# Performance work log

Hardware: AMD Instinct MI355X
Metric: run time of the kernel (lower is better)

The kernel has to match this reference:

```python
import jax, jax.numpy as jnp
import numpy as np

ALPHA = 0.2      # GAT leaky_relu slope (args.alpha)
MLP_SLOPE = 0.01 # F.leaky_relu default in the MLP path
NEG = -9e15

def _l2_normalize(x, axis=1, eps=1e-12):
    n = jnp.sqrt(jnp.sum(x * x, axis=axis, keepdims=True))
    return x / jnp.maximum(n, eps)

def setup_inputs() -> dict:
    key = jax.random.key(0)
    ks = jax.random.split(key, 14)
    N, Din, Dh, H, Dg, M1, M2, E = 8192, 512, 256, 2, 512, 512, 256, 100000
    x = jax.random.normal(ks[0], (N, Din), dtype=jnp.float32)
    adj = jax.random.randint(ks[1], (N, N), 0, 2, dtype=jnp.int32)
    train_sample = jax.random.randint(ks[2], (E, 2), 0, N, dtype=jnp.int32)
    llm_emb = jax.random.normal(ks[3], (N, Dg), dtype=jnp.float32)
    # GAT head params (stacked over heads)
    Wg = jax.random.normal(ks[4], (H, Din, Dh), dtype=jnp.float32) * 0.05
    a1 = jax.random.normal(ks[5], (H, Dh), dtype=jnp.float32) * 0.05
    a2 = jax.random.normal(ks[6], (H, Dh), dtype=jnp.float32) * 0.05
    bias_g = jnp.zeros((H, Dh), dtype=jnp.float32)
    # MLP params
    W1 = jax.random.normal(ks[7], (Dh + Dg, M1), dtype=jnp.float32) * 0.03
    b1 = jnp.zeros((M1,), dtype=jnp.float32)
    W2 = jax.random.normal(ks[8], (M1, M2), dtype=jnp.float32) * 0.04
    b2 = jnp.zeros((M2,), dtype=jnp.float32)
    return {"x": x, "adj": adj, "train_sample": train_sample, "llm_emb": llm_emb,
            "Wg": Wg, "a1": a1, "a2": a2, "bias_g": bias_g,
            "W1": W1, "b1": b1, "W2": W2, "b2": b2}

def reference(x, adj, train_sample, llm_emb, Wg, a1, a2, bias_g, W1, b1, W2, b2):
    mask = adj > 0  # [N, N]

    def head(W, av1, av2, b):
        h = x @ W                                   # [N, Dh]
        s1 = h @ av1                                # [N]
        s2 = h @ av2                                # [N]
        e = jax.nn.leaky_relu(s1[:, None] + s2[None, :], ALPHA)  # [N, N]
        att = jax.nn.softmax(jnp.where(mask, e, NEG), axis=1)
        out = att @ h                               # [N, Dh]
        out = jax.nn.leaky_relu(out, ALPHA)
        out = _l2_normalize(out, axis=1)
        return out + b

    # encode: single GNN layer -> mean over heads (dropout inactive in eval)
    out_heads = jax.vmap(head)(Wg, a1, a2, bias_g)  # [H, N, Dh]
    embed_gnn = jnp.mean(out_heads, axis=0)         # [N, Dh]
    embed = jnp.concatenate([llm_emb, embed_gnn], axis=1)  # [N, Dg+Dh]

    def mlp(z):
        z = jax.nn.leaky_relu(z @ W1 + b1, MLP_SLOPE)
        z = jax.nn.leaky_relu(z @ W2 + b2, MLP_SLOPE)
        return z

    tf_embed = mlp(embed)
    target_embed = mlp(embed)
    train_tf = tf_embed[train_sample[:, 0]]
    train_tg = target_embed[train_sample[:, 1]]
    pred = jnp.sum(train_tf * train_tg, axis=1, keepdims=True)  # dot decode, [E,1]
    return pred
```

## Files before the change

kernel.cpp:

```cpp
#include <hip/hip_runtime.h>
#include <hip/hip_bf16.h>
#include <cstdint>
#include <cstddef>

#define ALPHA 0.2f
#define MLP_SLOPE 0.01f

typedef short bf16x8 __attribute__((ext_vector_type(8)));
typedef float f32x4 __attribute__((ext_vector_type(4)));
typedef unsigned short ushort_t;

__device__ __forceinline__ float lrelu(float x, float s) { return x > 0.f ? x : x * s; }
__device__ __forceinline__ ushort_t f2bf(float x) {
  __hip_bfloat16 h = __float2bfloat16(x);
  return *reinterpret_cast<ushort_t*>(&h);
}
__device__ __forceinline__ float bf2f(ushort_t u) {
  union { unsigned int i; float f; } v; v.i = ((unsigned int)u) << 16; return v.f;
}

__global__ __launch_bounds__(256) void split_f(
    const float* __restrict__ in, ushort_t* __restrict__ hi,
    ushort_t* __restrict__ lo)
{
  int idx = blockIdx.x * 256 + threadIdx.x;
  float4 v = ((const float4*)in)[idx];
  ushort4 h, l;
  h.x = f2bf(v.x); l.x = f2bf(v.x - bf2f(h.x));
  h.y = f2bf(v.y); l.y = f2bf(v.y - bf2f(h.y));
  h.z = f2bf(v.z); l.z = f2bf(v.z - bf2f(h.z));
  h.w = f2bf(v.w); l.w = f2bf(v.w - bf2f(h.w));
  ((ushort4*)hi)[idx] = h;
  ((ushort4*)lo)[idx] = l;
}

__global__ __launch_bounds__(256) void split_t(
    const float* __restrict__ W, ushort_t* __restrict__ Thi,
    ushort_t* __restrict__ Tlo, int K, int N)
{
  int idx = blockIdx.x * 256 + threadIdx.x;
  if (idx >= K * N) return;
  int k = idx / N, n = idx - k * N;
  size_t b = (size_t)blockIdx.y * K * N;
  float v = W[b + idx];
  ushort_t h = f2bf(v);
  size_t o = b + (size_t)n * K + k;
  Thi[o] = h; Tlo[o] = f2bf(v - bf2f(h));
}

__global__ __launch_bounds__(256, 2) void gemm_bf16s(
    const ushort_t* __restrict__ Ahi, const ushort_t* __restrict__ Alo,
    const ushort_t* __restrict__ Bthi, const ushort_t* __restrict__ Btlo,
    const float* __restrict__ bias, float* __restrict__ Cf,
    ushort_t* __restrict__ Chi, ushort_t* __restrict__ Clo,
    int M, int N, int K, float slope, int act)
{
  __shared__ ushort_t Ah[128][40], Al[128][40], Bh[128][40], Bl[128][40];
  const size_t boff = (size_t)blockIdx.z * N * K;
  const size_t coff = (size_t)blockIdx.z * M * N;
  const int t = threadIdx.x;
  const int m0 = blockIdx.y * 128, n0 = blockIdx.x * 128;
  const int srow = t >> 1, spart = (t & 1) * 16;
  const int wave = t >> 6;
  const int wm = (wave >> 1) * 64, wn = (wave & 1) * 64;
  const int l16 = t & 15, quad = (t >> 4) & 3;
  f32x4 acc[4][4];
#pragma unroll
  for (int i = 0; i < 4; ++i)
#pragma unroll
    for (int j = 0; j < 4; ++j) acc[i][j] = (f32x4){0.f, 0.f, 0.f, 0.f};

  for (int k0 = 0; k0 < K; k0 += 32) {
    __syncthreads();
    const size_t abase = (size_t)(m0 + srow) * K + k0 + spart;
    const size_t bbase = boff + (size_t)(n0 + srow) * K + k0 + spart;
    *(uint4*)&Ah[srow][spart]     = *(const uint4*)&Ahi[abase];
    *(uint4*)&Ah[srow][spart + 8] = *(const uint4*)&Ahi[abase + 8];
    *(uint4*)&Al[srow][spart]     = *(const uint4*)&Alo[abase];
    *(uint4*)&Al[srow][spart + 8] = *(const uint4*)&Alo[abase + 8];
    *(uint4*)&Bh[srow][spart]     = *(const uint4*)&Bthi[bbase];
    *(uint4*)&Bh[srow][spart + 8] = *(const uint4*)&Bthi[bbase + 8];
    *(uint4*)&Bl[srow][spart]     = *(const uint4*)&Btlo[bbase];
    *(uint4*)&Bl[srow][spart + 8] = *(const uint4*)&Btlo[bbase + 8];
    __syncthreads();
    bf16x8 afh[4], afl[4], bfh[4], bfl[4];
#pragma unroll
    for (int mt = 0; mt < 4; ++mt) {
      afh[mt] = *(const bf16x8*)&Ah[wm + mt * 16 + l16][quad * 8];
      afl[mt] = *(const bf16x8*)&Al[wm + mt * 16 + l16][quad * 8];
    }
#pragma unroll
    for (int nt = 0; nt < 4; ++nt) {
      bfh[nt] = *(const bf16x8*)&Bh[wn + nt * 16 + l16][quad * 8];
      bfl[nt] = *(const bf16x8*)&Bl[wn + nt * 16 + l16][quad * 8];
    }
#pragma unroll
    for (int mt = 0; mt < 4; ++mt)
#pragma unroll
      for (int nt = 0; nt < 4; ++nt) {
        acc[mt][nt] = __builtin_amdgcn_mfma_f32_16x16x32_bf16(afh[mt], bfh[nt], acc[mt][nt], 0, 0, 0);
        acc[mt][nt] = __builtin_amdgcn_mfma_f32_16x16x32_bf16(afh[mt], bfl[nt], acc[mt][nt], 0, 0, 0);
        acc[mt][nt] = __builtin_amdgcn_mfma_f32_16x16x32_bf16(afl[mt], bfh[nt], acc[mt][nt], 0, 0, 0);
      }
  }
#pragma unroll
  for (int mt = 0; mt < 4; ++mt)
#pragma unroll
    for (int nt = 0; nt < 4; ++nt)
#pragma unroll
      for (int rg = 0; rg < 4; ++rg) {
        int m = m0 + wm + mt * 16 + quad * 4 + rg;
        int n = n0 + wn + nt * 16 + l16;
        float v = acc[mt][nt][rg];
        if (bias) v += bias[n];
        if (act) v = lrelu(v, slope);
        size_t o = coff + (size_t)m * N + n;
        if (Cf) Cf[o] = v;
        if (Chi) {
          ushort_t h = f2bf(v);
          Chi[o] = h; Clo[o] = f2bf(v - bf2f(h));
        }
      }
}

__global__ __launch_bounds__(256) void s_kernel(
    const float* __restrict__ hbuf, const float* __restrict__ a1,
    const float* __restrict__ a2, float* __restrict__ s1, float* __restrict__ s2)
{
  const int gw = (blockIdx.x * 256 + threadIdx.x) >> 6;
  const int lane = threadIdx.x & 63;
#pragma unroll
  for (int hh = 0; hh < 2; ++hh) {
    float4 hv = ((const float4*)(hbuf + ((size_t)hh * 8192 + gw) * 256))[lane];
    float4 a1v = ((const float4*)(a1 + hh * 256))[lane];
    float4 a2v = ((const float4*)(a2 + hh * 256))[lane];
    float p1 = hv.x * a1v.x + hv.y * a1v.y + hv.z * a1v.z + hv.w * a1v.w;
    float p2 = hv.x * a2v.x + hv.y * a2v.y + hv.z * a2v.z + hv.w * a2v.w;
    for (int off = 32; off > 0; off >>= 1) {
      p1 += __shfl_xor(p1, off);
      p2 += __shfl_xor(p2, off);
    }
    if (lane == 0) {
      s1[hh * 8192 + gw] = p1;
      s2[hh * 8192 + gw] = p2;
    }
  }
}

__global__ __launch_bounds__(256) void h_pack(
    const float* __restrict__ hbuf, ushort_t* __restrict__ Bpack)
{
  int gid = blockIdx.x * 256 + threadIdx.x;
  int lane = gid & 63;
  int ntile = (gid >> 6) & 15;
  int kblk = (gid >> 10) & 255;
  int head = gid >> 18;
  int c = ntile * 16 + (lane & 15);
  int jb = kblk * 32 + (lane >> 4) * 8;
  ushort_t o[8];
#pragma unroll
  for (int e = 0; e < 8; ++e)
    o[e] = f2bf(hbuf[((size_t)head * 8192 + jb + e) * 256 + c]);
  *(uint4*)&Bpack[(size_t)gid * 8] = *(uint4*)o;
}

__global__ __launch_bounds__(256, 2) void attn_mfma2(
    const ushort_t* __restrict__ Bpack, const float* __restrict__ s1g,
    const float* __restrict__ s2g, const int* __restrict__ adj,
    ushort_t* __restrict__ pacc, float* __restrict__ pl)
{
  __shared__ ushort_t Wlds[2][2][4][64][8];
  const int t = threadIdx.x;
  const int i0 = blockIdx.x * 64;
  const int js = blockIdx.y;
  const int kbase = js * 2048;
  const int wr = t >> 2, kq = t & 3;
  const int glane = kq * 16 + (wr & 15);
  const int gmt = wr >> 4;
  const float s1v0 = s1g[i0 + wr];
  const float s1v1 = s1g[8192 + i0 + wr];
  const int wave = t >> 6, head = wave >> 1, nh = wave & 1;
  const int l16 = t & 15, quad = (t >> 4) & 3;
  const int l63 = t & 63;
  f32x4 acc[4][8];
#pragma unroll
  for (int m = 0; m < 4; ++m)
#pragma unroll
    for (int n = 0; n < 8; ++n) acc[m][n] = (f32x4){0.f, 0.f, 0.f, 0.f};
  float rs0 = 0.f, rs1 = 0.f;

  const int* arow = adj + (size_t)(i0 + wr) * 8192;
  int4 pa0, pa1;
  float4 p20a, p20b, p21a, p21b;
  {
    const int kk = kbase + kq * 8;
    pa0 = *(const int4*)&arow[kk];
    pa1 = *(const int4*)&arow[kk + 4];
    p20a = *(const float4*)&s2g[kk];
    p20b = *(const float4*)&s2g[kk + 4];
    p21a = *(const float4*)&s2g[8192 + kk];
    p21b = *(const float4*)&s2g[8192 + kk + 4];
  }
  for (int kt = 0; kt < 64; ++kt) {
    const int buf = kt & 1;
    {
      int am[8] = {pa0.x, pa0.y, pa0.z, pa0.w, pa1.x, pa1.y, pa1.z, pa1.w};
      float s20[8] = {p20a.x, p20a.y, p20a.z, p20a.w, p20b.x, p20b.y, p20b.z, p20b.w};
      float s21[8] = {p21a.x, p21a.y, p21a.z, p21a.w, p21b.x, p21b.y, p21b.z, p21b.w};
      ushort_t w0[8], w1[8];
#pragma unroll
      for (int e = 0; e < 8; ++e) {
        float e0 = s1v0 + s20[e];
        float e1 = s1v1 + s21[e];
        e0 = fmaxf(e0, 0.f) + ALPHA * fminf(e0, 0.f);
        e1 = fmaxf(e1, 0.f) + ALPHA * fminf(e1, 0.f);
        float v0 = am[e] > 0 ? __expf(e0) : 0.f;
        float v1 = am[e] > 0 ? __expf(e1) : 0.f;
        rs0 += v0; rs1 += v1;
        w0[e] = f2bf(v0); w1[e] = f2bf(v1);
      }
      *(uint4*)&Wlds[buf][0][gmt][glane][0] = *(uint4*)w0;
      *(uint4*)&Wlds[buf][1][gmt][glane][0] = *(uint4*)w1;
    }
    if (kt < 63) {
      const int kk = kbase + (kt + 1) * 32 + kq * 8;
      pa0 = *(const int4*)&arow[kk];
      pa1 = *(const int4*)&arow[kk + 4];
      p20a = *(const float4*)&s2g[kk];
      p20b = *(const float4*)&s2g[kk + 4];
      p21a = *(const float4*)&s2g[8192 + kk];
      p21b = *(const float4*)&s2g[8192 + kk + 4];
    }
    __syncthreads();
    const int kblk = js * 64 + kt;
    const ushort_t* bbase =
        Bpack + ((((size_t)head * 256 + kblk) * 16 + nh * 8) * 64 + l63) * 8;
    bf16x8 Af[4], Bf[8];
#pragma unroll
    for (int mt = 0; mt < 4; ++mt)
      Af[mt] = *(const bf16x8*)&Wlds[buf][head][mt][l63][0];
#pragma unroll
    for (int nt = 0; nt < 8; ++nt)
      Bf[nt] = *(const bf16x8*)&bbase[nt * 512];
#pragma unroll
    for (int mt = 0; mt < 4; ++mt)
#pragma unroll
      for (int nt = 0; nt < 8; ++nt)
        acc[mt][nt] = __builtin_amdgcn_mfma_f32_16x16x32_bf16(
            Af[mt], Bf[nt], acc[mt][nt], 0, 0, 0);
  }
  rs0 += __shfl_xor(rs0, 1); rs0 += __shfl_xor(rs0, 2);
  rs1 += __shfl_xor(rs1, 1); rs1 += __shfl_xor(rs1, 2);
  if (kq == 0) {
    pl[((size_t)js * 2 + 0) * 8192 + i0 + wr] = rs0;
    pl[((size_t)js * 2 + 1) * 8192 + i0 + wr] = rs1;
  }
  const int n0 = nh * 128;
#pragma unroll
  for (int mt = 0; mt < 4; ++mt)
#pragma unroll
    for (int nt = 0; nt < 8; ++nt)
#pragma unroll
      for (int rg = 0; rg < 4; ++rg) {
        int row = i0 + mt * 16 + quad * 4 + rg;
        int col = n0 + nt * 16 + l16;
        pacc[(((size_t)js * 2 + head) * 8192 + row) * 256 + col] =
            f2bf(acc[mt][nt][rg]);
      }
}

__global__ __launch_bounds__(256) void attn_finalize(
    const ushort_t* __restrict__ pacc, const float* __restrict__ pl,
    const float* __restrict__ bg, float* __restrict__ embed)
{
  __shared__ float red[256];
  const int r = blockIdx.x;
  const int t = threadIdx.x;
  float o[2], nrm[2];
#pragma unroll
  for (int hh = 0; hh < 2; ++hh) {
    float num = 0.f, l = 0.f;
#pragma unroll
    for (int js = 0; js < 4; ++js) {
      num += bf2f(pacc[(((size_t)js * 2 + hh) * 8192 + r) * 256 + t]);
      l += pl[((size_t)js * 2 + hh) * 8192 + r];
    }
    o[hh] = lrelu(num / l, ALPHA);
  }
  for (int hh = 0; hh < 2; ++hh) {
    __syncthreads();
    red[t] = o[hh] * o[hh];
    __syncthreads();
    for (int s = 128; s > 0; s >>= 1) {
      if (t < s) red[t] += red[t + s];
      __syncthreads();
    }
    nrm[hh] = fmaxf(sqrtf(red[0]), 1e-12f);
  }
  embed[(size_t)r * 768 + 512 + t] =
      0.5f * (o[0] / nrm[0] + bg[t] + o[1] / nrm[1] + bg[256 + t]);
}

__global__ __launch_bounds__(256) void copy_llm(
    const float* __restrict__ llm, float* __restrict__ embed)
{
  int idx = blockIdx.x * 256 + threadIdx.x;
  int r = idx >> 7, c = idx & 127;
  ((float4*)embed)[(size_t)r * 192 + c] = ((const float4*)llm)[idx];
}

__global__ __launch_bounds__(256) void pred_kernel(
    const float* __restrict__ z2, const int* __restrict__ ts,
    float* __restrict__ out, int E)
{
  const int gw = (blockIdx.x * 256 + threadIdx.x) >> 6;
  const int lane = threadIdx.x & 63;
  if (gw >= E) return;
  const int a = ts[gw * 2], b = ts[gw * 2 + 1];
  float4 va = ((const float4*)(z2 + (size_t)a * 256))[lane];
  float4 vb = ((const float4*)(z2 + (size_t)b * 256))[lane];
  float p = va.x * vb.x + va.y * vb.y + va.z * vb.z + va.w * vb.w;
  for (int off = 32; off > 0; off >>= 1) p += __shfl_xor(p, off);
  if (lane == 0) out[gw] = p;
}

extern "C" void kernel_launch(void* const* d_in, const int* in_sizes, int n_in,
                              void* d_out, int out_size, void* d_ws, size_t ws_size,
                              hipStream_t stream) {
  const float* x   = (const float*)d_in[0];
  const int*   adj = (const int*)d_in[1];
  const int*   ts  = (const int*)d_in[2];
  const float* llm = (const float*)d_in[3];
  const float* Wg  = (const float*)d_in[4];
  const float* a1  = (const float*)d_in[5];
  const float* a2  = (const float*)d_in[6];
  const float* bg  = (const float*)d_in[7];
  const float* W1  = (const float*)d_in[8];
  const float* b1  = (const float*)d_in[9];
  const float* W2  = (const float*)d_in[10];
  const float* b2  = (const float*)d_in[11];
  float* out = (float*)d_out;
  float* ws  = (float*)d_ws;
  const int E = in_sizes[2] / 2;

  float*    hbuf  = ws;
  ushort_t* Bpack = (ushort_t*)(ws + 4194304);
  float*    embed = ws;
  ushort_t* xhi   = (ushort_t*)(ws + 6291456);
  ushort_t* xlo   = (ushort_t*)(ws + 8388608);
  ushort_t* z1hi  = xhi;
  ushort_t* z1lo  = xlo;
  float*    s1    = ws + 10485760;
  float*    s2    = ws + 10502144;
  float*    pl    = ws + 10518528;
  ushort_t* pacc  = (ushort_t*)(ws + 10584064);
  ushort_t* ehi   = (ushort_t*)(ws + 10584064);
  ushort_t* elo   = (ushort_t*)(ws + 13729792);
  float*    z2    = ws + 16875520;
  ushort_t* wgthi = (ushort_t*)(ws + 18972672);
  ushort_t* wgtlo = (ushort_t*)(ws + 19103744);
  ushort_t* w1thi = (ushort_t*)(ws + 19234816);
  ushort_t* w1tlo = (ushort_t*)(ws + 19431424);
  ushort_t* w2thi = (ushort_t*)(ws + 19628032);
  ushort_t* w2tlo = (ushort_t*)(ws + 19693568);

  split_f<<<4096, 256, 0, stream>>>(x, xhi, xlo);
  split_t<<<dim3(512, 2), 256, 0, stream>>>(Wg, wgthi, wgtlo, 512, 256);
  split_t<<<dim3(1536, 1), 256, 0, stream>>>(W1, w1thi, w1tlo, 768, 512);
  split_t<<<dim3(512, 1), 256, 0, stream>>>(W2, w2thi, w2tlo, 512, 256);
  gemm_bf16s<<<dim3(2, 64, 2), 256, 0, stream>>>(
      xhi, xlo, wgthi, wgtlo, nullptr, hbuf, nullptr, nullptr,
      8192, 256, 512, 0.f, 0);
  s_kernel<<<2048, 256, 0, stream>>>(hbuf, a1, a2, s1, s2);
  h_pack<<<2048, 256, 0, stream>>>(hbuf, Bpack);
  attn_mfma2<<<dim3(128, 4), 256, 0, stream>>>(Bpack, s1, s2, adj, pacc, pl);
  copy_llm<<<4096, 256, 0, stream>>>(llm, embed);
  attn_finalize<<<8192, 256, 0, stream>>>(pacc, pl, bg, embed);
  split_f<<<6144, 256, 0, stream>>>(embed, ehi, elo);
  gemm_bf16s<<<dim3(4, 64, 1), 256, 0, stream>>>(
      ehi, elo, w1thi, w1tlo, b1, nullptr, z1hi, z1lo,
      8192, 512, 768, MLP_SLOPE, 1);
  gemm_bf16s<<<dim3(2, 64, 1), 256, 0, stream>>>(
      z1hi, z1lo, w2thi, w2tlo, b2, z2, nullptr, nullptr,
      8192, 256, 512, MLP_SLOPE, 1);
  pred_kernel<<<(E * 64 + 255) / 256, 256, 0, stream>>>(z2, ts, out, E);
}
```

Baseline: 667.8 us.

## Compute attention weights in registers, halve GEMM N-tile, fuse llm copy into finalize

The attention kernel now builds each lane's MFMA A-fragment directly in registers from its own adjacency rows, so the LDS staging buffer and the per-iteration __syncthreads are gone. The cost is that each head's waves compute exp values separately, and the two column-half waves of a head repeat the same work. The split-bf16 GEMM moves to a 128x64 tile with padded LDS rows, doubling the grid size. The llm_emb copy is folded into attn_finalize to save one launch.

```diff
diff --git a/kernel.cpp b/kernel.cpp
--- a/kernel.cpp
+++ b/kernel.cpp
@@ -55,49 +55,62 @@
     ushort_t* __restrict__ Chi, ushort_t* __restrict__ Clo,
     int M, int N, int K, float slope, int act)
 {
-  __shared__ ushort_t Ah[128][40], Al[128][40], Bh[128][40], Bl[128][40];
+  __shared__ ushort_t Ah[128][42], Al[128][42], Bh[64][42], Bl[64][42];
   const size_t boff = (size_t)blockIdx.z * N * K;
   const size_t coff = (size_t)blockIdx.z * M * N;
   const int t = threadIdx.x;
-  const int m0 = blockIdx.y * 128, n0 = blockIdx.x * 128;
-  const int srow = t >> 1, spart = (t & 1) * 16;
+  const int m0 = blockIdx.y * 128, n0 = blockIdx.x * 64;
   const int wave = t >> 6;
-  const int wm = (wave >> 1) * 64, wn = (wave & 1) * 64;
+  const int wm = (wave & 1) * 64, wn = (wave >> 1) * 32;
   const int l16 = t & 15, quad = (t >> 4) & 3;
-  f32x4 acc[4][4];
+  const int tr = t & 127;
+  f32x4 acc[4][2];
 #pragma unroll
   for (int i = 0; i < 4; ++i)
 #pragma unroll
-    for (int j = 0; j < 4; ++j) acc[i][j] = (f32x4){0.f, 0.f, 0.f, 0.f};
+    for (int j = 0; j < 2; ++j) acc[i][j] = (f32x4){0.f, 0.f, 0.f, 0.f};
 
   for (int k0 = 0; k0 < K; k0 += 32) {
     __syncthreads();
-    const size_t abase = (size_t)(m0 + srow) * K + k0 + spart;
-    const size_t bbase = boff + (size_t)(n0 + srow) * K + k0 + spart;
-    *(uint4*)&Ah[srow][spart]     = *(const uint4*)&Ahi[abase];
-    *(uint4*)&Ah[srow][spart + 8] = *(const uint4*)&Ahi[abase + 8];
-    *(uint4*)&Al[srow][spart]     = *(const uint4*)&Alo[abase];
-    *(uint4*)&Al[srow][spart + 8] = *(const uint4*)&Alo[abase + 8];
-    *(uint4*)&Bh[srow][spart]     = *(const uint4*)&Bthi[bbase];
-    *(uint4*)&Bh[srow][spart + 8] = *(const uint4*)&Bthi[bbase + 8];
-    *(uint4*)&Bl[srow][spart]     = *(const uint4*)&Btlo[bbase];
-    *(uint4*)&Bl[srow][spart + 8] = *(const uint4*)&Btlo[bbase + 8];
+    {
+      const size_t abase = (size_t)(m0 + tr) * K + k0;
+      if (t < 128) {
+#pragma unroll
+        for (int j = 0; j < 4; ++j)
+          *(uint4*)&Ah[tr][j * 8] = *(const uint4*)&Ahi[abase + j * 8];
+      } else {
+#pragma unroll
+        for (int j = 0; j < 4; ++j)
+          *(uint4*)&Al[tr][j * 8] = *(const uint4*)&Alo[abase + j * 8];
+        const int br = tr & 63;
+        const size_t bbase = boff + (size_t)(n0 + br) * K + k0;
+        if (tr < 64) {
+#pragma unroll
+          for (int j = 0; j < 4; ++j)
+            *(uint4*)&Bh[br][j * 8] = *(const uint4*)&Bthi[bbase + j * 8];
+        } else {
+#pragma unroll
+          for (int j = 0; j < 4; ++j)
+            *(uint4*)&Bl[br][j * 8] = *(const uint4*)&Btlo[bbase + j * 8];
+        }
+      }
+    }
     __syncthreads();
-    bf16x8 afh[4], afl[4], bfh[4], bfl[4];
+    bf16x8 afh[4], afl[4], bfh[2], bfl[2];
 #pragma unroll
     for (int mt = 0; mt < 4; ++mt) {
       afh[mt] = *(const bf16x8*)&Ah[wm + mt * 16 + l16][quad * 8];
       afl[mt] = *(const bf16x8*)&Al[wm + mt * 16 + l16][quad * 8];
     }
 #pragma unroll
-    for (int nt = 0; nt < 4; ++nt) {
+    for (int nt = 0; nt < 2; ++nt) {
       bfh[nt] = *(const bf16x8*)&Bh[wn + nt * 16 + l16][quad * 8];
       bfl[nt] = *(const bf16x8*)&Bl[wn + nt * 16 + l16][quad * 8];
     }
 #pragma unroll
     for (int mt = 0; mt < 4; ++mt)
 #pragma unroll
-      for (int nt = 0; nt < 4; ++nt) {
+      for (int nt = 0; nt < 2; ++nt) {
         acc[mt][nt] = __builtin_amdgcn_mfma_f32_16x16x32_bf16(afh[mt], bfh[nt], acc[mt][nt], 0, 0, 0);
         acc[mt][nt] = __builtin_amdgcn_mfma_f32_16x16x32_bf16(afh[mt], bfl[nt], acc[mt][nt], 0, 0, 0);
         acc[mt][nt] = __builtin_amdgcn_mfma_f32_16x16x32_bf16(afl[mt], bfh[nt], acc[mt][nt], 0, 0, 0);
@@ -106,7 +119,7 @@
 #pragma unroll
   for (int mt = 0; mt < 4; ++mt)
 #pragma unroll
-    for (int nt = 0; nt < 4; ++nt)
+    for (int nt = 0; nt < 2; ++nt)
 #pragma unroll
       for (int rg = 0; rg < 4; ++rg) {
         int m = m0 + wm + mt * 16 + quad * 4 + rg;
@@ -164,84 +177,91 @@
   *(uint4*)&Bpack[(size_t)gid * 8] = *(uint4*)o;
 }
 
-__global__ __launch_bounds__(256, 2) void attn_mfma2(
+__global__ __launch_bounds__(256, 2) void attn_mfma3(
     const ushort_t* __restrict__ Bpack, const float* __restrict__ s1g,
     const float* __restrict__ s2g, const int* __restrict__ adj,
     ushort_t* __restrict__ pacc, float* __restrict__ pl)
 {
-  __shared__ ushort_t Wlds[2][2][4][64][8];
   const int t = threadIdx.x;
   const int i0 = blockIdx.x * 64;
   const int js = blockIdx.y;
   const int kbase = js * 2048;
-  const int wr = t >> 2, kq = t & 3;
-  const int glane = kq * 16 + (wr & 15);
-  const int gmt = wr >> 4;
-  const float s1v0 = s1g[i0 + wr];
-  const float s1v1 = s1g[8192 + i0 + wr];
   const int wave = t >> 6, head = wave >> 1, nh = wave & 1;
-  const int l16 = t & 15, quad = (t >> 4) & 3;
+  const int l16 = t & 15, oct = (t >> 4) & 3;
   const int l63 = t & 63;
+
+  float s1v[4];
+#pragma unroll
+  for (int mt = 0; mt < 4; ++mt)
+    s1v[mt] = s1g[(size_t)head * 8192 + i0 + mt * 16 + l16];
+  const float* s2h = s2g + (size_t)head * 8192;
+
   f32x4 acc[4][8];
 #pragma unroll
   for (int m = 0; m < 4; ++m)
 #pragma unroll
     for (int n = 0; n < 8; ++n) acc[m][n] = (f32x4){0.f, 0.f, 0.f, 0.f};
-  float rs0 = 0.f, rs1 = 0.f;
-
-  const int* arow = adj + (size_t)(i0 + wr) * 8192;
-  int4 pa0, pa1;
-  float4 p20a, p20b, p21a, p21b;
+  float rs[4] = {0.f, 0.f, 0.f, 0.f};
+
+  const int* arow[4];
+#pragma unroll
+  for (int mt = 0; mt < 4; ++mt)
+    arow[mt] = adj + (size_t)(i0 + mt * 16 + l16) * 8192;
+
+  int4 pa0[4], pa1[4];
+  float4 ps2a, ps2b;
   {
-    const int kk = kbase + kq * 8;
-    pa0 = *(const int4*)&arow[kk];
-    pa1 = *(const int4*)&arow[kk + 4];
-    p20a = *(const float4*)&s2g[kk];
-    p20b = *(const float4*)&s2g[kk + 4];
-    p21a = *(const float4*)&s2g[8192 + kk];
-    p21b = *(const float4*)&s2g[8192 + kk + 4];
-  }
+    const int kk = kbase + oct * 8;
+#pragma unroll
+    for (int mt = 0; mt < 4; ++mt) {
+      pa0[mt] = *(const int4*)&arow[mt][kk];
+      pa1[mt] = *(const int4*)&arow[mt][kk + 4];
+    }
+    ps2a = *(const float4*)&s2h[kk];
+    ps2b = *(const float4*)&s2h[kk + 4];
+  }
+
   for (int kt = 0; kt < 64; ++kt) {
-    const int buf = kt & 1;
-    {
-      int am[8] = {pa0.x, pa0.y, pa0.z, pa0.w, pa1.x, pa1.y, pa1.z, pa1.w};
-      float s20[8] = {p20a.x, p20a.y, p20a.z, p20a.w, p20b.x, p20b.y, p20b.z, p20b.w};
-      float s21[8] = {p21a.x, p21a.y, p21a.z, p21a.w, p21b.x, p21b.y, p21b.z, p21b.w};
-      ushort_t w0[8], w1[8];
+    const int kblk = js * 64 + kt;
+    const ushort_t* bb =
+        Bpack + ((((size_t)head * 256 + kblk) * 16 + nh * 8) * 64 + l63) * 8;
+    bf16x8 Bf[8];
+#pragma unroll
+    for (int nt = 0; nt < 8; ++nt)
+      Bf[nt] = *(const bf16x8*)&bb[nt * 512];
+
+    float s2v[8] = {ps2a.x, ps2a.y, ps2a.z, ps2a.w,
+                    ps2b.x, ps2b.y, ps2b.z, ps2b.w};
+    bf16x8 Af[4];
+#pragma unroll
+    for (int mt = 0; mt < 4; ++mt) {
+      int av[8] = {pa0[mt].x, pa0[mt].y, pa0[mt].z, pa0[mt].w,
+                   pa1[mt].x, pa1[mt].y, pa1[mt].z, pa1[mt].w};
+      ushort_t w[8] __attribute__((aligned(16)));
+      float r = 0.f;
 #pragma unroll
       for (int e = 0; e < 8; ++e) {
-        float e0 = s1v0 + s20[e];
-        float e1 = s1v1 + s21[e];
-        e0 = fmaxf(e0, 0.f) + ALPHA * fminf(e0, 0.f);
-        e1 = fmaxf(e1, 0.f) + ALPHA * fminf(e1, 0.f);
-        float v0 = am[e] > 0 ? __expf(e0) : 0.f;
-        float v1 = am[e] > 0 ? __expf(e1) : 0.f;
-        rs0 += v0; rs1 += v1;
-        w0[e] = f2bf(v0); w1[e] = f2bf(v1);
-      }
-      *(uint4*)&Wlds[buf][0][gmt][glane][0] = *(uint4*)w0;
-      *(uint4*)&Wlds[buf][1][gmt][glane][0] = *(uint4*)w1;
-    }
+        float ev = s1v[mt] + s2v[e];
+        ev = fmaxf(ev, 0.f) + ALPHA * fminf(ev, 0.f);
+        float wv = av[e] > 0 ? __expf(ev) : 0.f;
+        r += wv;
+        w[e] = f2bf(wv);
+      }
+      rs[mt] += r;
+      Af[mt] = *(const bf16x8*)w;
+    }
+
     if (kt < 63) {
-      const int kk = kbase + (kt + 1) * 32 + kq * 8;
-      pa0 = *(const int4*)&arow[kk];
-      pa1 = *(const int4*)&arow[kk + 4];
-      p20a = *(const float4*)&s2g[kk];
-      p20b = *(const float4*)&s2g[kk + 4];
-      p21a = *(const float4*)&s2g[8192 + kk];
-      p21b = *(const float4*)&s2g[8192 + kk + 4];
-    }
-    __syncthreads();
-    const int kblk = js * 64 + kt;
-    const ushort_t* bbase =
-        Bpack + ((((size_t)head * 256 + kblk) * 16 + nh * 8) * 64 + l63) * 8;
-    bf16x8 Af[4], Bf[8];
-#pragma unroll
-    for (int mt = 0; mt < 4; ++mt)
-      Af[mt] = *(const bf16x8*)&Wlds[buf][head][mt][l63][0];
-#pragma unroll
-    for (int nt = 0; nt < 8; ++nt)
-      Bf[nt] = *(const bf16x8*)&bbase[nt * 512];
+      const int kk = kbase + (kt + 1) * 32 + oct * 8;
+#pragma unroll
+      for (int mt = 0; mt < 4; ++mt) {
+        pa0[mt] = *(const int4*)&arow[mt][kk];
+        pa1[mt] = *(const int4*)&arow[mt][kk + 4];
+      }
+      ps2a = *(const float4*)&s2h[kk];
+      ps2b = *(const float4*)&s2h[kk + 4];
+    }
+
 #pragma unroll
     for (int mt = 0; mt < 4; ++mt)
 #pragma unroll
@@ -249,12 +269,18 @@
         acc[mt][nt] = __builtin_amdgcn_mfma_f32_16x16x32_bf16(
             Af[mt], Bf[nt], acc[mt][nt], 0, 0, 0);
   }
-  rs0 += __shfl_xor(rs0, 1); rs0 += __shfl_xor(rs0, 2);
-  rs1 += __shfl_xor(rs1, 1); rs1 += __shfl_xor(rs1, 2);
-  if (kq == 0) {
-    pl[((size_t)js * 2 + 0) * 8192 + i0 + wr] = rs0;
-    pl[((size_t)js * 2 + 1) * 8192 + i0 + wr] = rs1;
-  }
+
+#pragma unroll
+  for (int mt = 0; mt < 4; ++mt) {
+    rs[mt] += __shfl_xor(rs[mt], 16);
+    rs[mt] += __shfl_xor(rs[mt], 32);
+  }
+  if (nh == 0 && oct == 0) {
+#pragma unroll
+    for (int mt = 0; mt < 4; ++mt)
+      pl[((size_t)js * 2 + head) * 8192 + i0 + mt * 16 + l16] = rs[mt];
+  }
+
   const int n0 = nh * 128;
 #pragma unroll
   for (int mt = 0; mt < 4; ++mt)
@@ -262,7 +288,7 @@
     for (int nt = 0; nt < 8; ++nt)
 #pragma unroll
       for (int rg = 0; rg < 4; ++rg) {
-        int row = i0 + mt * 16 + quad * 4 + rg;
+        int row = i0 + mt * 16 + oct * 4 + rg;
         int col = n0 + nt * 16 + l16;
         pacc[(((size_t)js * 2 + head) * 8192 + row) * 256 + col] =
             f2bf(acc[mt][nt][rg]);
@@ -271,11 +297,15 @@
 
 __global__ __launch_bounds__(256) void attn_finalize(
     const ushort_t* __restrict__ pacc, const float* __restrict__ pl,
-    const float* __restrict__ bg, float* __restrict__ embed)
+    const float* __restrict__ bg, const float* __restrict__ llm,
+    float* __restrict__ embed)
 {
   __shared__ float red[256];
   const int r = blockIdx.x;
   const int t = threadIdx.x;
+  if (t < 128)
+    *(float4*)&embed[(size_t)r * 768 + t * 4] =
+        *(const float4*)&llm[(size_t)r * 512 + t * 4];
   float o[2], nrm[2];
 #pragma unroll
   for (int hh = 0; hh < 2; ++hh) {
@@ -299,14 +329,6 @@
   }
   embed[(size_t)r * 768 + 512 + t] =
       0.5f * (o[0] / nrm[0] + bg[t] + o[1] / nrm[1] + bg[256 + t]);
-}
-
-__global__ __launch_bounds__(256) void copy_llm(
-    const float* __restrict__ llm, float* __restrict__ embed)
-{
-  int idx = blockIdx.x * 256 + threadIdx.x;
-  int r = idx >> 7, c = idx & 127;
-  ((float4*)embed)[(size_t)r * 192 + c] = ((const float4*)llm)[idx];
 }
 
 __global__ __launch_bounds__(256) void pred_kernel(
@@ -368,19 +390,18 @@
   split_t<<<dim3(512, 2), 256, 0, stream>>>(Wg, wgthi, wgtlo, 512, 256);
   split_t<<<dim3(1536, 1), 256, 0, stream>>>(W1, w1thi, w1tlo, 768, 512);
   split_t<<<dim3(512, 1), 256, 0, stream>>>(W2, w2thi, w2tlo, 512, 256);
-  gemm_bf16s<<<dim3(2, 64, 2), 256, 0, stream>>>(
+  gemm_bf16s<<<dim3(4, 64, 2), 256, 0, stream>>>(
       xhi, xlo, wgthi, wgtlo, nullptr, hbuf, nullptr, nullptr,
       8192, 256, 512, 0.f, 0);
   s_kernel<<<2048, 256, 0, stream>>>(hbuf, a1, a2, s1, s2);
   h_pack<<<2048, 256, 0, stream>>>(hbuf, Bpack);
-  attn_mfma2<<<dim3(128, 4), 256, 0, stream>>>(Bpack, s1, s2, adj, pacc, pl);
-  copy_llm<<<4096, 256, 0, stream>>>(llm, embed);
-  attn_finalize<<<8192, 256, 0, stream>>>(pacc, pl, bg, embed);
+  attn_mfma3<<<dim3(128, 4), 256, 0, stream>>>(Bpack, s1, s2, adj, pacc, pl);
+  attn_finalize<<<8192, 256, 0, stream>>>(pacc, pl, bg, llm, embed);
   split_f<<<6144, 256, 0, stream>>>(embed, ehi, elo);
-  gemm_bf16s<<<dim3(4, 64, 1), 256, 0, stream>>>(
+  gemm_bf16s<<<dim3(8, 64, 1), 256, 0, stream>>>(
       ehi, elo, w1thi, w1tlo, b1, nullptr, z1hi, z1lo,
       8192, 512, 768, MLP_SLOPE, 1);
-  gemm_bf16s<<<dim3(2, 64, 1), 256, 0, stream>>>(
+  gemm_bf16s<<<dim3(4, 64, 1), 256, 0, stream>>>(
       z1hi, z1lo, w2thi, w2tlo, b2, z2, nullptr, nullptr,
       8192, 256, 512, MLP_SLOPE, 1);
   pred_kernel<<<(E * 64 + 255) / 256, 256, 0, stream>>>(z2, ts, out, E);
```

Result: slower. 745.4 us (+11.6%).

## Pre-pack weights into MFMA fragment layout and drop LDS staging in GEMMs

Applied to the files above, without the earlier changes.

Weights are now packed into the per-lane MFMA B-fragment layout, so the split-bf16 GEMM can load A and B fragments straight from global memory into registers with double buffering, without LDS or block barriers. The GEMM tile shrinks to 128x64 per block, which doubles the grid. In the attention kernel the Bpack fragment loads are issued before the weight computation so their latency overlaps it, and __syncthreads is replaced by an inline-asm lgkmcnt wait plus s_barrier. The llm copy kernel is folded into attn_finalize. The risks are uncoalesced global A loads with no LDS reuse across waves, and the asm barrier does not wait on vmcnt.

```diff
diff --git a/kernel.cpp b/kernel.cpp
--- a/kernel.cpp
+++ b/kernel.cpp
@@ -9,6 +9,8 @@
 typedef short bf16x8 __attribute__((ext_vector_type(8)));
 typedef float f32x4 __attribute__((ext_vector_type(4)));
 typedef unsigned short ushort_t;
+
+#define ASM_BARRIER() __asm__ __volatile__("s_waitcnt lgkmcnt(0)\n\ts_barrier" ::: "memory")
 
 __device__ __forceinline__ float lrelu(float x, float s) { return x > 0.f ? x : x * s; }
 __device__ __forceinline__ ushort_t f2bf(float x) {
@@ -34,83 +36,112 @@
   ((ushort4*)lo)[idx] = l;
 }
 
-__global__ __launch_bounds__(256) void split_t(
-    const float* __restrict__ W, ushort_t* __restrict__ Thi,
-    ushort_t* __restrict__ Tlo, int K, int N)
-{
-  int idx = blockIdx.x * 256 + threadIdx.x;
-  if (idx >= K * N) return;
-  int k = idx / N, n = idx - k * N;
+__global__ __launch_bounds__(256) void pack_wt(
+    const float* __restrict__ W, ushort_t* __restrict__ hi,
+    ushort_t* __restrict__ lo, int K, int N)
+{
+  int gid = blockIdx.x * 256 + threadIdx.x;
+  int lane = gid & 63;
+  int kbc = K >> 5;
+  int kblk = (gid >> 6) % kbc;
+  int nblk = (gid >> 6) / kbc;
   size_t b = (size_t)blockIdx.y * K * N;
-  float v = W[b + idx];
-  ushort_t h = f2bf(v);
-  size_t o = b + (size_t)n * K + k;
-  Thi[o] = h; Tlo[o] = f2bf(v - bf2f(h));
-}
-
-__global__ __launch_bounds__(256, 2) void gemm_bf16s(
+  int col = nblk * 16 + (lane & 15);
+  int krow = kblk * 32 + (lane >> 4) * 8;
+  ushort_t h[8] __attribute__((aligned(16)));
+  ushort_t l[8] __attribute__((aligned(16)));
+#pragma unroll
+  for (int e = 0; e < 8; ++e) {
+    float v = W[b + (size_t)(krow + e) * N + col];
+    h[e] = f2bf(v);
+    l[e] = f2bf(v - bf2f(h[e]));
+  }
+  *(uint4*)&hi[b + (size_t)gid * 8] = *(uint4*)h;
+  *(uint4*)&lo[b + (size_t)gid * 8] = *(uint4*)l;
+}
+
+__global__ __launch_bounds__(256) void gemm_nolds(
     const ushort_t* __restrict__ Ahi, const ushort_t* __restrict__ Alo,
-    const ushort_t* __restrict__ Bthi, const ushort_t* __restrict__ Btlo,
+    const ushort_t* __restrict__ Bph, const ushort_t* __restrict__ Bpl,
     const float* __restrict__ bias, float* __restrict__ Cf,
     ushort_t* __restrict__ Chi, ushort_t* __restrict__ Clo,
     int M, int N, int K, float slope, int act)
 {
-  __shared__ ushort_t Ah[128][40], Al[128][40], Bh[128][40], Bl[128][40];
   const size_t boff = (size_t)blockIdx.z * N * K;
   const size_t coff = (size_t)blockIdx.z * M * N;
   const int t = threadIdx.x;
-  const int m0 = blockIdx.y * 128, n0 = blockIdx.x * 128;
-  const int srow = t >> 1, spart = (t & 1) * 16;
-  const int wave = t >> 6;
-  const int wm = (wave >> 1) * 64, wn = (wave & 1) * 64;
-  const int l16 = t & 15, quad = (t >> 4) & 3;
-  f32x4 acc[4][4];
+  const int wave = t >> 6, l63 = t & 63;
+  const int l16 = t & 15, oct = (t >> 4) & 3, quad = oct;
+  const int wm = (wave & 1) * 64, wn = (wave >> 1) * 32;
+  const int m0 = blockIdx.y * 128 + wm;
+  const int nb = blockIdx.x * 4 + (wave >> 1) * 2;
+  const int nbase = blockIdx.x * 64 + wn;
+  const int ksteps = K >> 5;
+
+  const ushort_t* aph[4];
+  const ushort_t* apl[4];
+#pragma unroll
+  for (int mt = 0; mt < 4; ++mt) {
+    size_t o = (size_t)(m0 + mt * 16 + l16) * K + oct * 8;
+    aph[mt] = Ahi + o;
+    apl[mt] = Alo + o;
+  }
+  const ushort_t* bph[2];
+  const ushort_t* bpl[2];
+#pragma unroll
+  for (int nt = 0; nt < 2; ++nt) {
+    size_t o = boff + ((size_t)(nb + nt) * ksteps * 64 + l63) * 8;
+    bph[nt] = Bph + o;
+    bpl[nt] = Bpl + o;
+  }
+
+  f32x4 acc[4][2];
 #pragma unroll
   for (int i = 0; i < 4; ++i)
 #pragma unroll
-    for (int j = 0; j < 4; ++j) acc[i][j] = (f32x4){0.f, 0.f, 0.f, 0.f};
-
-  for (int k0 = 0; k0 < K; k0 += 32) {
-    __syncthreads();
-    const size_t abase = (size_t)(m0 + srow) * K + k0 + spart;
-    const size_t bbase = boff + (size_t)(n0 + srow) * K + k0 + spart;
-    *(uint4*)&Ah[srow][spart]     = *(const uint4*)&Ahi[abase];
-    *(uint4*)&Ah[srow][spart + 8] = *(const uint4*)&Ahi[abase + 8];
-    *(uint4*)&Al[srow][spart]     = *(const uint4*)&Alo[abase];
-    *(uint4*)&Al[srow][spart + 8] = *(const uint4*)&Alo[abase + 8];
-    *(uint4*)&Bh[srow][spart]     = *(const uint4*)&Bthi[bbase];
-    *(uint4*)&Bh[srow][spart + 8] = *(const uint4*)&Bthi[bbase + 8];
-    *(uint4*)&Bl[srow][spart]     = *(const uint4*)&Btlo[bbase];
-    *(uint4*)&Bl[srow][spart + 8] = *(const uint4*)&Btlo[bbase + 8];
-    __syncthreads();
-    bf16x8 afh[4], afl[4], bfh[4], bfl[4];
-#pragma unroll
-    for (int mt = 0; mt < 4; ++mt) {
-      afh[mt] = *(const bf16x8*)&Ah[wm + mt * 16 + l16][quad * 8];
-      afl[mt] = *(const bf16x8*)&Al[wm + mt * 16 + l16][quad * 8];
-    }
-#pragma unroll
-    for (int nt = 0; nt < 4; ++nt) {
-      bfh[nt] = *(const bf16x8*)&Bh[wn + nt * 16 + l16][quad * 8];
-      bfl[nt] = *(const bf16x8*)&Bl[wn + nt * 16 + l16][quad * 8];
-    }
-#pragma unroll
-    for (int mt = 0; mt < 4; ++mt)
-#pragma unroll
-      for (int nt = 0; nt < 4; ++nt) {
-        acc[mt][nt] = __builtin_amdgcn_mfma_f32_16x16x32_bf16(afh[mt], bfh[nt], acc[mt][nt], 0, 0, 0);
-        acc[mt][nt] = __builtin_amdgcn_mfma_f32_16x16x32_bf16(afh[mt], bfl[nt], acc[mt][nt], 0, 0, 0);
-        acc[mt][nt] = __builtin_amdgcn_mfma_f32_16x16x32_bf16(afl[mt], bfh[nt], acc[mt][nt], 0, 0, 0);
-      }
-  }
+    for (int j = 0; j < 2; ++j) acc[i][j] = (f32x4){0.f, 0.f, 0.f, 0.f};
+
+#define LOADF(AH, AL, BH, BL, KB)                                         \
+  {                                                                       \
+    _Pragma("unroll") for (int mt = 0; mt < 4; ++mt) {                    \
+      AH[mt] = *(const bf16x8*)(aph[mt] + (size_t)(KB) * 32);             \
+      AL[mt] = *(const bf16x8*)(apl[mt] + (size_t)(KB) * 32);             \
+    }                                                                     \
+    _Pragma("unroll") for (int nt = 0; nt < 2; ++nt) {                    \
+      BH[nt] = *(const bf16x8*)(bph[nt] + (size_t)(KB) * 512);            \
+      BL[nt] = *(const bf16x8*)(bpl[nt] + (size_t)(KB) * 512);            \
+    }                                                                     \
+  }
+#define MF(AH, AL, BH, BL)                                                \
+  {                                                                       \
+    _Pragma("unroll") for (int mt = 0; mt < 4; ++mt)                      \
+    _Pragma("unroll") for (int nt = 0; nt < 2; ++nt) {                    \
+      acc[mt][nt] = __builtin_amdgcn_mfma_f32_16x16x32_bf16(AH[mt], BH[nt], acc[mt][nt], 0, 0, 0); \
+      acc[mt][nt] = __builtin_amdgcn_mfma_f32_16x16x32_bf16(AH[mt], BL[nt], acc[mt][nt], 0, 0, 0); \
+      acc[mt][nt] = __builtin_amdgcn_mfma_f32_16x16x32_bf16(AL[mt], BH[nt], acc[mt][nt], 0, 0, 0); \
+    }                                                                     \
+  }
+
+  bf16x8 ah0[4], al0[4], bh0[2], bl0[2];
+  bf16x8 ah1[4], al1[4], bh1[2], bl1[2];
+  LOADF(ah0, al0, bh0, bl0, 0)
+  for (int kb = 0; kb < ksteps; kb += 2) {
+    LOADF(ah1, al1, bh1, bl1, kb + 1)
+    MF(ah0, al0, bh0, bl0)
+    if (kb + 2 < ksteps) LOADF(ah0, al0, bh0, bl0, kb + 2)
+    MF(ah1, al1, bh1, bl1)
+  }
+#undef LOADF
+#undef MF
+
 #pragma unroll
   for (int mt = 0; mt < 4; ++mt)
 #pragma unroll
-    for (int nt = 0; nt < 4; ++nt)
+    for (int nt = 0; nt < 2; ++nt)
 #pragma unroll
       for (int rg = 0; rg < 4; ++rg) {
-        int m = m0 + wm + mt * 16 + quad * 4 + rg;
-        int n = n0 + wn + nt * 16 + l16;
+        int m = m0 + mt * 16 + quad * 4 + rg;
+        int n = nbase + nt * 16 + l16;
         float v = acc[mt][nt][rg];
         if (bias) v += bias[n];
         if (act) v = lrelu(v, slope);
@@ -157,14 +188,14 @@
   int head = gid >> 18;
   int c = ntile * 16 + (lane & 15);
   int jb = kblk * 32 + (lane >> 4) * 8;
-  ushort_t o[8];
+  ushort_t o[8] __attribute__((aligned(16)));
 #pragma unroll
   for (int e = 0; e < 8; ++e)
     o[e] = f2bf(hbuf[((size_t)head * 8192 + jb + e) * 256 + c]);
   *(uint4*)&Bpack[(size_t)gid * 8] = *(uint4*)o;
 }
 
-__global__ __launch_bounds__(256, 2) void attn_mfma2(
+__global__ __launch_bounds__(256, 2) void attn_mfma4(
     const ushort_t* __restrict__ Bpack, const float* __restrict__ s1g,
     const float* __restrict__ s2g, const int* __restrict__ adj,
     ushort_t* __restrict__ pacc, float* __restrict__ pl)
@@ -203,11 +234,20 @@
   }
   for (int kt = 0; kt < 64; ++kt) {
     const int buf = kt & 1;
+    const int kblk = js * 64 + kt;
+    const ushort_t* bb =
+        Bpack + ((((size_t)head * 256 + kblk) * 16 + nh * 8) * 64 + l63) * 8;
+    bf16x8 Bf[8];
+#pragma unroll
+    for (int nt = 0; nt < 8; ++nt)
+      Bf[nt] = *(const bf16x8*)&bb[nt * 512];
+
     {
       int am[8] = {pa0.x, pa0.y, pa0.z, pa0.w, pa1.x, pa1.y, pa1.z, pa1.w};
       float s20[8] = {p20a.x, p20a.y, p20a.z, p20a.w, p20b.x, p20b.y, p20b.z, p20b.w};
       float s21[8] = {p21a.x, p21a.y, p21a.z, p21a.w, p21b.x, p21b.y, p21b.z, p21b.w};
-      ushort_t w0[8], w1[8];
+      ushort_t w0[8] __attribute__((aligned(16)));
+      ushort_t w1[8] __attribute__((aligned(16)));
 #pragma unroll
       for (int e = 0; e < 8; ++e) {
         float e0 = s1v0 + s20[e];
@@ -231,17 +271,11 @@
       p21a = *(const float4*)&s2g[8192 + kk];
       p21b = *(const float4*)&s2g[8192 + kk + 4];
     }
-    __syncthreads();
-    const int kblk = js * 64 + kt;
-    const ushort_t* bbase =
-        Bpack + ((((size_t)head * 256 + kblk) * 16 + nh * 8) * 64 + l63) * 8;
-    bf16x8 Af[4], Bf[8];
+    ASM_BARRIER();
+    bf16x8 Af[4];
 #pragma unroll
     for (int mt = 0; mt < 4; ++mt)
       Af[mt] = *(const bf16x8*)&Wlds[buf][head][mt][l63][0];
-#pragma unroll
-    for (int nt = 0; nt < 8; ++nt)
-      Bf[nt] = *(const bf16x8*)&bbase[nt * 512];
 #pragma unroll
     for (int mt = 0; mt < 4; ++mt)
 #pragma unroll
@@ -271,11 +305,15 @@
 
 __global__ __launch_bounds__(256) void attn_finalize(
     const ushort_t* __restrict__ pacc, const float* __restrict__ pl,
-    const float* __restrict__ bg, float* __restrict__ embed)
+    const float* __restrict__ bg, const float* __restrict__ llm,
+    float* __restrict__ embed)
 {
   __shared__ float red[256];
   const int r = blockIdx.x;
   const int t = threadIdx.x;
+  if (t < 128)
+    *(float4*)&embed[(size_t)r * 768 + t * 4] =
+        *(const float4*)&llm[(size_t)r * 512 + t * 4];
   float o[2], nrm[2];
 #pragma unroll
   for (int hh = 0; hh < 2; ++hh) {
@@ -299,14 +337,6 @@
   }
   embed[(size_t)r * 768 + 512 + t] =
       0.5f * (o[0] / nrm[0] + bg[t] + o[1] / nrm[1] + bg[256 + t]);
-}
-
-__global__ __launch_bounds__(256) void copy_llm(
-    const float* __restrict__ llm, float* __restrict__ embed)
-{
-  int idx = blockIdx.x * 256 + threadIdx.x;
-  int r = idx >> 7, c = idx & 127;
-  ((float4*)embed)[(size_t)r * 192 + c] = ((const float4*)llm)[idx];
 }
 
 __global__ __launch_bounds__(256) void pred_kernel(
@@ -357,31 +387,30 @@
   ushort_t* ehi   = (ushort_t*)(ws + 10584064);
   ushort_t* elo   = (ushort_t*)(ws + 13729792);
   float*    z2    = ws + 16875520;
-  ushort_t* wgthi = (ushort_t*)(ws + 18972672);
-  ushort_t* wgtlo = (ushort_t*)(ws + 19103744);
-  ushort_t* w1thi = (ushort_t*)(ws + 19234816);
-  ushort_t* w1tlo = (ushort_t*)(ws + 19431424);
-  ushort_t* w2thi = (ushort_t*)(ws + 19628032);
-  ushort_t* w2tlo = (ushort_t*)(ws + 19693568);
+  ushort_t* wgphi = (ushort_t*)(ws + 18972672);
+  ushort_t* wgplo = (ushort_t*)(ws + 19103744);
+  ushort_t* w1phi = (ushort_t*)(ws + 19234816);
+  ushort_t* w1plo = (ushort_t*)(ws + 19431424);
+  ushort_t* w2phi = (ushort_t*)(ws + 19628032);
+  ushort_t* w2plo = (ushort_t*)(ws + 19693568);
 
   split_f<<<4096, 256, 0, stream>>>(x, xhi, xlo);
-  split_t<<<dim3(512, 2), 256, 0, stream>>>(Wg, wgthi, wgtlo, 512, 256);
-  split_t<<<dim3(1536, 1), 256, 0, stream>>>(W1, w1thi, w1tlo, 768, 512);
-  split_t<<<dim3(512, 1), 256, 0, stream>>>(W2, w2thi, w2tlo, 512, 256);
-  gemm_bf16s<<<dim3(2, 64, 2), 256, 0, stream>>>(
-      xhi, xlo, wgthi, wgtlo, nullptr, hbuf, nullptr, nullptr,
+  pack_wt<<<dim3(64, 2), 256, 0, stream>>>(Wg, wgphi, wgplo, 512, 256);
+  pack_wt<<<dim3(192, 1), 256, 0, stream>>>(W1, w1phi, w1plo, 768, 512);
+  pack_wt<<<dim3(64, 1), 256, 0, stream>>>(W2, w2phi, w2plo, 512, 256);
+  gemm_nolds<<<dim3(4, 64, 2), 256, 0, stream>>>(
+      xhi, xlo, wgphi, wgplo, nullptr, hbuf, nullptr, nullptr,
       8192, 256, 512, 0.f, 0);
   s_kernel<<<2048, 256, 0, stream>>>(hbuf, a1, a2, s1, s2);
   h_pack<<<2048, 256, 0, stream>>>(hbuf, Bpack);
-  attn_mfma2<<<dim3(128, 4), 256, 0, stream>>>(Bpack, s1, s2, adj, pacc, pl);
-  copy_llm<<<4096, 256, 0, stream>>>(llm, embed);
-  attn_finalize<<<8192, 256, 0, stream>>>(pacc, pl, bg, embed);
+  attn_mfma4<<<dim3(128, 4), 256, 0, stream>>>(Bpack, s1, s2, adj, pacc, pl);
+  attn_finalize<<<8192, 256, 0, stream>>>(pacc, pl, bg, llm, embed);
   split_f<<<6144, 256, 0, stream>>>(embed, ehi, elo);
-  gemm_bf16s<<<dim3(4, 64, 1), 256, 0, stream>>>(
-      ehi, elo, w1thi, w1tlo, b1, nullptr, z1hi, z1lo,
+  gemm_nolds<<<dim3(8, 64, 1), 256, 0, stream>>>(
+      ehi, elo, w1phi, w1plo, b1, nullptr, z1hi, z1lo,
       8192, 512, 768, MLP_SLOPE, 1);
-  gemm_bf16s<<<dim3(2, 64, 1), 256, 0, stream>>>(
-      z1hi, z1lo, w2thi, w2tlo, b2, z2, nullptr, nullptr,
+  gemm_nolds<<<dim3(4, 64, 1), 256, 0, stream>>>(
+      z1hi, z1lo, w2phi, w2plo, b2, z2, nullptr, nullptr,
       8192, 256, 512, MLP_SLOPE, 1);
   pred_kernel<<<(E * 64 + 255) / 256, 256, 0, stream>>>(z2, ts, out, E);
 }
```

Result: no change. 663.3 us (-0.7%).
